# Performance work log

Hardware: AMD Instinct MI355X
Metric: run time of the kernel (lower is better)

## Reference

```python
import jax, jax.numpy as jnp
import numpy as np

NOISE_EPS = 1e-2   # Shazeer noisy-gating stddev floor
LN_EPS = 1e-6
LOSS_COEF = 0.01
K = 2              # num_activated_experts


def _layer_norm(x, w, b):
    mu = jnp.mean(x, axis=-1, keepdims=True)
    var = jnp.var(x, axis=-1, keepdims=True)
    return (x - mu) * jax.lax.rsqrt(var + LN_EPS) * w + b


def _cv_squared(v):
    return jnp.var(v) / (jnp.mean(v) ** 2 + 1e-10)


def _normal_cdf(z):
    return 0.5 * (1.0 + jax.scipy.special.erf(z / jnp.sqrt(jnp.asarray(2.0, z.dtype))))


def setup_inputs() -> dict:
    key = jax.random.key(0)
    ks = jax.random.split(key, 8)
    N, D, H, O, E = 8192, 512, 1024, 512, 8
    x = jax.random.normal(ks[0], (N, D), jnp.float32)
    x_offsets = jnp.sort(jax.random.randint(ks[1], (17,), 0, N)).astype(jnp.int64)
    noise = jax.random.normal(ks[2], (N, E), jnp.float32)
    s = 0.02
    return {
        "x": x,
        "x_offsets": x_offsets,
        "max_seq_len": 2048,
        "noise": noise,
        "norm_w": jnp.ones((D,), jnp.float32),
        "norm_bias": jnp.zeros((D,), jnp.float32),
        "w_gate": jax.random.normal(ks[3], (D, E), jnp.float32) * s,
        "w_noise": jax.random.normal(ks[4], (D, E), jnp.float32) * s,
        "W1": jax.random.normal(ks[5], (E, H, D), jnp.float32) * s,  # [E, model_d, input]
        "b1": jnp.zeros((E, H), jnp.float32),
        "W2": jax.random.normal(ks[6], (E, O, H), jnp.float32) * s,  # [E, output, model_d]
        "b2": jnp.zeros((E, O), jnp.float32),
        "output_weight": jax.random.normal(ks[7], (D, O), jnp.float32) * s,
    }


def reference(x, x_offsets, max_seq_len, noise, norm_w, norm_bias, w_gate, w_noise,
              W1, b1, W2, b2, output_weight):
    N, D = x.shape
    E = w_gate.shape[1]
    k_plus = min(K + 1, E)

    # pre-norm
    x_norm = _layer_norm(x, norm_w, norm_bias)

    # noisy top-k gating (training path)
    clean_logits = x_norm @ w_gate                      # [N, E]
    noise_stddev = jax.nn.softplus(x_norm @ w_noise) + NOISE_EPS
    noisy_logits = clean_logits + noise * noise_stddev

    top_logits, top_indices = jax.lax.top_k(noisy_logits, k_plus)   # [N, k+1]
    top_k_logits = top_logits[:, :K]
    top_k_indices = top_indices[:, :K]
    top_k_gates = jax.nn.softmax(top_k_logits, axis=-1)             # [N, K]

    rows = jnp.arange(N)[:, None]
    gates = jnp.zeros((N, E), top_k_gates.dtype).at[rows, top_k_indices].set(top_k_gates)

    # load = prob each expert is in top-k under the gating noise (Shazeer)
    flat = top_logits.reshape(-1)
    pos_in = jnp.arange(N) * k_plus + K
    thr_in = flat[pos_in][:, None]          # (k+1)-th value: threshold if already in
    thr_out = flat[pos_in - 1][:, None]     # k-th value: threshold if currently out
    is_in = noisy_logits > thr_in
    prob_in = _normal_cdf((clean_logits - thr_in) / noise_stddev)
    prob_out = _normal_cdf((clean_logits - thr_out) / noise_stddev)
    load_probs = jnp.where(is_in, prob_in, prob_out)                # [N, E]

    loss = LOSS_COEF * (_cv_squared(gates.sum(0)) + _cv_squared(load_probs.sum(0)))

    # dispatch stats: tokens per expert
    lengths = jnp.zeros((E,), jnp.float32).at[top_k_indices.reshape(-1)].add(1.0)
    load = lengths / lengths.sum()

    # grouped expert MLP (dense one-hot combine; gates are 0 for unrouted experts)
    h = jnp.einsum('nd,ehd->neh', x_norm, W1) + b1                  # [N, E, H]
    a = jax.nn.silu(h)
    y_e = jnp.einsum('neh,eoh->neo', a, W2) + b2                    # [N, E, O]
    y_moe = jnp.einsum('ne,neo->no', gates, y_e)                    # [N, O]

    # shared expert: addmm(y, shared_x=x, output_weight)
    y = y_moe + x @ output_weight
    return y, loss, load
```

## Files before the change

### kernel.cpp

```cpp
#include <hip/hip_runtime.h>
#include <math.h>

typedef unsigned short u16;
typedef unsigned int u32;

#define N_ROWS 8192
#define DDIM 512
#define HDIM 1024
#define ODIM 512
#define NEXP 8
#define MAXPAIRS (N_ROWS * 2)
#define MAXPOS (MAXPAIRS + NEXP * 128)
#define MAXTILES (MAXPOS / 128)

#define SM_CNT 0
#define SM_CUR 8
#define SM_AOFF 16
#define SM_GSUM 32
#define SM_LSUM 40
#define SM_WORDS 64

using short8 = __attribute__((ext_vector_type(8))) short;
using float4v = __attribute__((ext_vector_type(4))) float;

__device__ __forceinline__ u16 f2bf(float f) {
    union { float f; u32 u; } v; v.f = f;
    u32 u = v.u;
    return (u16)((u + 0x7fffu + ((u >> 16) & 1u)) >> 16);
}

__device__ __forceinline__ void async_copy16(u16* lds, const u16* g) {
    __builtin_amdgcn_global_load_lds(
        (const __attribute__((address_space(1))) void*)g,
        (__attribute__((address_space(3))) void*)lds, 16, 0, 0);
}

__global__ __launch_bounds__(512) void init1_kernel(int* small, float* zeropage) {
    int i = threadIdx.x;
    if (i < SM_WORDS) small[i] = 0;
    zeropage[i] = 0.f;
}

#define W1CONV_BLOCKS 4096
#define OWT_BLOCKS 256
#define BUCKET_BLOCKS 68
#define W2CONV_BLOCKS 2048
__global__ __launch_bounds__(256) void prep_kernel(
    const float* __restrict__ W1, const float* __restrict__ ow,
    const float* __restrict__ W2,
    u16* __restrict__ W1b, u16* __restrict__ owT, u16* __restrict__ W2b,
    int* __restrict__ bucket_rows)
{
    __shared__ __align__(16) float tile[32][33];
    int cb = blockIdx.x, tid = threadIdx.x;
    if (cb < W1CONV_BLOCKS) {
        size_t i = (size_t)cb * 256 + tid;
        float4 v = ((const float4*)W1)[i];
        ushort4 o;
        o.x = f2bf(v.x); o.y = f2bf(v.y); o.z = f2bf(v.z); o.w = f2bf(v.w);
        ((ushort4*)W1b)[i] = o;
    } else if (cb < W1CONV_BLOCKS + OWT_BLOCKS) {
        int t = cb - W1CONV_BLOCKS;
        int bx = (t & 15) * 32, by = (t >> 4) * 32;
        int tx = tid & 31, ty = tid >> 5;
        for (int r = ty; r < 32; r += 8) tile[r][tx] = ow[(size_t)(by + r) * ODIM + bx + tx];
        __syncthreads();
        for (int r = ty; r < 32; r += 8) owT[(size_t)(bx + r) * DDIM + by + tx] = f2bf(tile[tx][r]);
    } else if (cb < W1CONV_BLOCKS + OWT_BLOCKS + BUCKET_BLOCKS) {
        int i = (cb - W1CONV_BLOCKS - OWT_BLOCKS) * 256 + tid;
        if (i < MAXPOS) bucket_rows[i] = -1;
    } else {
        int j = cb - W1CONV_BLOCKS - OWT_BLOCKS - BUCKET_BLOCKS;
        size_t i = (size_t)j * 512 + tid;
#pragma unroll
        for (int t = 0; t < 2; t++, i += 256) {
            float4 v = ((const float4*)W2)[i];
            ushort4 o;
            o.x = f2bf(v.x); o.y = f2bf(v.y); o.z = f2bf(v.z); o.w = f2bf(v.w);
            ((ushort4*)W2b)[i] = o;
        }
    }
}

#define GATE_BLOCKS 512
__global__ __launch_bounds__(256) void gate_kernel(
    const float* __restrict__ x, const float* __restrict__ noise,
    const float* __restrict__ norm_w, const float* __restrict__ norm_b,
    const float* __restrict__ w_gate, const float* __restrict__ w_noise,
    u16* __restrict__ xnorm_bf, u16* __restrict__ x_bf,
    int* __restrict__ pair_expert, float* __restrict__ pair_gate,
    int* __restrict__ small)
{
    __shared__ __align__(16) float sh[2 * NEXP * DDIM + 16 * 17 + 32];
    float* wgT = sh;
    float* wnT = sh + NEXP * DDIM;
    float* lg = sh + 2 * NEXP * DDIM;
    float* blk_g = lg + 16 * 17;
    float* blk_l = blk_g + NEXP;
    int* blk_c = (int*)(blk_l + NEXP);
    float* smf = (float*)small;

    int b = blockIdx.x, tid = threadIdx.x;
    for (int i = tid; i < NEXP * DDIM; i += 256) {
        int d = i >> 3, e = i & 7;
        wgT[e * DDIM + d] = w_gate[i];
        wnT[e * DDIM + d] = w_noise[i];
    }
    if (tid < NEXP) { blk_g[tid] = 0.f; blk_l[tid] = 0.f; blk_c[tid] = 0; }
    __syncthreads();

    int wave = tid >> 6, lane = tid & 63;
    float nw[8], nb[8];
#pragma unroll
    for (int j = 0; j < 8; j++) { nw[j] = norm_w[j * 64 + lane]; nb[j] = norm_b[j * 64 + lane]; }

    bool l5 = (lane & 32) != 0, l4 = (lane & 16) != 0;
    bool l3 = (lane & 8) != 0, l2 = (lane & 4) != 0;

    for (int r = 0; r < 4; ++r) {
        int lrow16 = wave * 4 + r;
        int row = b * 16 + lrow16;
        const float* xr = x + (size_t)row * DDIM;
        float xv[8], s = 0.f, s2 = 0.f;
#pragma unroll
        for (int j = 0; j < 8; j++) { float v = xr[j * 64 + lane]; xv[j] = v; s += v; s2 += v * v; }
#pragma unroll
        for (int o = 32; o; o >>= 1) { s += __shfl_xor(s, o, 64); s2 += __shfl_xor(s2, o, 64); }
        float mu = s * (1.f / DDIM);
        float var = s2 * (1.f / DDIM) - mu * mu;
        float rstd = rsqrtf(var + 1e-6f);

        float acc[16];
#pragma unroll
        for (int e = 0; e < 16; e++) acc[e] = 0.f;
#pragma unroll
        for (int j = 0; j < 8; j++) {
            float v = (xv[j] - mu) * rstd * nw[j] + nb[j];
            int d = j * 64 + lane;
            xnorm_bf[(size_t)row * DDIM + d] = f2bf(v);
            x_bf[(size_t)row * DDIM + d] = f2bf(xv[j]);
#pragma unroll
            for (int e = 0; e < 8; e++) {
                acc[e] += v * wgT[e * DDIM + d];
                acc[8 + e] += v * wnT[e * DDIM + d];
            }
        }
        float t8[8];
#pragma unroll
        for (int v = 0; v < 8; v++) {
            float snd = l5 ? acc[v] : acc[v + 8];
            float kp = l5 ? acc[v + 8] : acc[v];
            t8[v] = kp + __shfl_xor(snd, 32, 64);
        }
        float t4[4];
#pragma unroll
        for (int v = 0; v < 4; v++) {
            float snd = l4 ? t8[v] : t8[v + 4];
            float kp = l4 ? t8[v + 4] : t8[v];
            t4[v] = kp + __shfl_xor(snd, 16, 64);
        }
        float t2[2];
#pragma unroll
        for (int v = 0; v < 2; v++) {
            float snd = l3 ? t4[v] : t4[v + 2];
            float kp = l3 ? t4[v + 2] : t4[v];
            t2[v] = kp + __shfl_xor(snd, 8, 64);
        }
        {
            float snd = l2 ? t2[0] : t2[1];
            float kp = l2 ? t2[1] : t2[0];
            float t1 = kp + __shfl_xor(snd, 4, 64);
            t1 += __shfl_xor(t1, 2, 64);
            t1 += __shfl_xor(t1, 1, 64);
            if ((lane & 3) == 0) lg[lrow16 * 17 + ((lane >> 2) & 15)] = t1;
        }
    }
    __syncthreads();

    if (tid < 16) {
        int row = b * 16 + tid;
        float cl[8], sd[8], nz[8];
#pragma unroll
        for (int e = 0; e < 8; e++) {
            cl[e] = lg[tid * 17 + e];
            float t = lg[tid * 17 + 8 + e];
            float sp = fmaxf(t, 0.f) + log1pf(expf(-fabsf(t)));
            sd[e] = sp + 0.01f;
            nz[e] = cl[e] + noise[(size_t)row * NEXP + e] * sd[e];
        }
        int idx[3]; float val[3]; u32 msk = 0;
#pragma unroll
        for (int t = 0; t < 3; t++) {
            float best = -INFINITY; int bi = 0;
#pragma unroll
            for (int e = 0; e < 8; e++)
                if (!((msk >> e) & 1) && nz[e] > best) { best = nz[e]; bi = e; }
            idx[t] = bi; val[t] = best; msk |= 1u << bi;
        }
        float e1 = expf(val[1] - val[0]);
        float g0 = 1.f / (1.f + e1), g1 = e1 / (1.f + e1);
        float thr_in = val[2], thr_out = val[1];

        pair_expert[row * 2] = idx[0]; pair_gate[row * 2] = g0;
        pair_expert[row * 2 + 1] = idx[1]; pair_gate[row * 2 + 1] = g1;
        atomicAdd(&blk_g[idx[0]], g0); atomicAdd(&blk_g[idx[1]], g1);
        atomicAdd(&blk_c[idx[0]], 1); atomicAdd(&blk_c[idx[1]], 1);
#pragma unroll
        for (int e = 0; e < 8; e++) {
            float thr = (nz[e] > thr_in) ? thr_in : thr_out;
            float z = (cl[e] - thr) / sd[e];
            float p = 0.5f * (1.f + erff(z * 0.70710678118654752f));
            atomicAdd(&blk_l[e], p);
        }
    }
    __syncthreads();
    if (tid < NEXP) {
        atomicAdd(smf + SM_GSUM + tid, blk_g[tid]);
        atomicAdd(smf + SM_LSUM + tid, blk_l[tid]);
        atomicAdd(&small[SM_CNT + tid], blk_c[tid]);
    }
}

__global__ __launch_bounds__(256) void scatter_kernel(
    const int* __restrict__ pair_expert, const float* __restrict__ pair_gate,
    int* __restrict__ small, int* __restrict__ bucket_rows, float* __restrict__ gate_by_pos,
    int* __restrict__ rowpos,
    float* __restrict__ out_loss, float* __restrict__ out_load)
{
    __shared__ int aoff[NEXP + 1];
    __shared__ int blk_cnt[NEXP];
    __shared__ int blk_base[NEXP];
    int tid = threadIdx.x;
    if (tid == 0) {
        int acc = 0; aoff[0] = 0;
        for (int e = 0; e < NEXP; e++) { acc += (small[SM_CNT + e] + 127) & ~127; aoff[e + 1] = acc; }
    }
    if (tid < NEXP) blk_cnt[tid] = 0;
    __syncthreads();
    int p = blockIdx.x * 256 + tid;
    int e = pair_expert[p];
    int local = atomicAdd(&blk_cnt[e], 1);
    __syncthreads();
    if (tid < NEXP)
        blk_base[tid] = aoff[tid] + atomicAdd(&small[SM_CUR + tid], blk_cnt[tid]);
    if (blockIdx.x == 0 && tid < NEXP + 1) small[SM_AOFF + tid] = aoff[tid];
    __syncthreads();
    int pos = blk_base[e] + local;
    bucket_rows[pos] = p >> 1;
    gate_by_pos[pos] = pair_gate[p];
    rowpos[p] = pos;

    if (blockIdx.x == 0 && tid == 0) {
        const float* gs = (const float*)small + SM_GSUM;
        const float* ls = (const float*)small + SM_LSUM;
        float cv[2];
        for (int t = 0; t < 2; t++) {
            const float* v = t ? ls : gs;
            float m = 0.f;
            for (int k = 0; k < NEXP; k++) m += v[k];
            m *= (1.f / NEXP);
            float var = 0.f;
            for (int k = 0; k < NEXP; k++) { float d = v[k] - m; var += d * d; }
            var *= (1.f / NEXP);
            cv[t] = var / (m * m + 1e-10f);
        }
        out_loss[0] = 0.01f * (cv[0] + cv[1]);
        int tot = 0;
        for (int k = 0; k < NEXP; k++) tot += small[SM_CNT + k];
        float inv = 1.f / (float)tot;
        for (int k = 0; k < NEXP; k++) out_load[k] = (float)small[SM_CNT + k] * inv;
    }
}

__global__ __launch_bounds__(256) void gemmA_kernel(
    const u16* __restrict__ xnorm, const u16* __restrict__ W1b,
    const u16* __restrict__ xbf, const u16* __restrict__ owT,
    const int* __restrict__ bucket_rows, const int* __restrict__ small,
    const float* __restrict__ b1, const u16* __restrict__ zeropage,
    u16* __restrict__ a_buf, float* __restrict__ y)
{
    constexpr int KD = 512;
    __shared__ __align__(16) u16 As[128 * 64];
    __shared__ __align__(16) u16 Bs[128 * 64];

    int tid = threadIdx.x;
    if (blockIdx.y >= 8) {
        int j = (blockIdx.y - 8) * 136 + blockIdx.x;
        if (j >= 256) return;
        int base = (j >> 2) * 128, bn = (j & 3) * 128;
        int wave = tid >> 6, lane = tid & 63;
        const int lrow = lane >> 2;
        const int kcol = (((lane & 3) ^ ((lane >> 3) & 3)) * 8);
        const int trow = wave * 32 + lrow;
        int wm = (wave & 1) * 64, wn = (wave >> 1) * 64;
        int fr = lane & 15, kq = lane >> 4;
        const int kg = ((kq ^ ((fr >> 1) & 3)) * 8);
        const u16* ga0 = xbf + (size_t)(base + trow) * KD + kcol;
        const u16* ga1 = xbf + (size_t)(base + trow + 16) * KD + kcol;
        const u16* gb0 = owT + (size_t)(bn + trow) * KD + kcol;
        const u16* gb1 = owT + (size_t)(bn + trow + 16) * KD + kcol;
        u16* As2 = (u16*)As; u16* Bs2 = (u16*)Bs;
        const int ofA0 = (wave * 32) * 32, ofA1 = (wave * 32 + 16) * 32;

        float4v acc[4][4];
#pragma unroll
        for (int i = 0; i < 4; i++)
#pragma unroll
            for (int jj = 0; jj < 4; jj++) acc[i][jj] = (float4v){0.f, 0.f, 0.f, 0.f};

        async_copy16(As2 + ofA0, ga0); async_copy16(As2 + ofA1, ga1);
        async_copy16(Bs2 + ofA0, gb0); async_copy16(Bs2 + ofA1, gb1);
        __syncthreads();
        int cur = 0;
        for (int t = 0; t < 16; ++t) {
            int nxt = cur ^ 1;
            if (t + 1 < 16) {
                int k1 = (t + 1) << 5;
                async_copy16(As2 + nxt * 4096 + ofA0, ga0 + k1);
                async_copy16(As2 + nxt * 4096 + ofA1, ga1 + k1);
                async_copy16(Bs2 + nxt * 4096 + ofA0, gb0 + k1);
                async_copy16(Bs2 + nxt * 4096 + ofA1, gb1 + k1);
            }
            short8 af[4], bf[4];
#pragma unroll
            for (int mt = 0; mt < 4; mt++) af[mt] = *(const short8*)&As2[cur * 4096 + (wm + mt * 16 + fr) * 32 + kg];
#pragma unroll
            for (int nt = 0; nt < 4; nt++) bf[nt] = *(const short8*)&Bs2[cur * 4096 + (wn + nt * 16 + fr) * 32 + kg];
#pragma unroll
            for (int mt = 0; mt < 4; mt++)
#pragma unroll
                for (int nt = 0; nt < 4; nt++)
                    acc[mt][nt] = __builtin_amdgcn_mfma_f32_16x16x32_bf16(af[mt], bf[nt], acc[mt][nt], 0, 0, 0);
            __syncthreads();
            cur = nxt;
        }
        int rbase = (lane >> 4) * 4, c16 = lane & 15;
#pragma unroll
        for (int mt = 0; mt < 4; mt++) {
            int gm = base + wm + mt * 16 + rbase;
#pragma unroll
            for (int nt = 0; nt < 4; nt++) {
                int gn = bn + wn + nt * 16 + c16;
#pragma unroll
                for (int r = 0; r < 4; r++)
                    y[(size_t)(gm + r) * ODIM + gn] = acc[mt][nt][r];
            }
        }
        return;
    }

    int base = blockIdx.x * 128;
    if (base >= small[SM_AOFF + 8]) return;
    int e = 0;
    while (e < 7 && base >= small[SM_AOFF + e + 1]) ++e;
    int bn = blockIdx.y * 128;
    const u16* Bsel = W1b + (size_t)e * HDIM * KD;

    int wave = tid >> 6, lane = tid & 63;
    int lr = lane >> 3;
    int lc = ((lane & 7) ^ lr) * 8;

    const u16* ga[4]; const u16* gb[4];
    u16* la[4]; u16* lb[4];
#pragma unroll
    for (int c = 0; c < 4; c++) {
        int tr = wave * 32 + c * 8;
        int r0 = bucket_rows[base + tr + lr];
        ga[c] = ((r0 < 0) ? zeropage : xnorm + (size_t)r0 * KD) + lc;
        gb[c] = Bsel + (size_t)(bn + tr + lr) * KD + lc;
        la[c] = &As[tr * 64];
        lb[c] = &Bs[tr * 64];
    }

    int wm = (wave & 1) * 64, wn = (wave >> 1) * 64;
    int fr = lane & 15, kq = lane >> 4, f7 = fr & 7;

    float4v acc[4][4];
#pragma unroll
    for (int i = 0; i < 4; i++)
#pragma unroll
        for (int j = 0; j < 4; j++) acc[i][j] = (float4v){0.f, 0.f, 0.f, 0.f};

    for (int k0 = 0; k0 < KD; k0 += 64) {
        __syncthreads();
#pragma unroll
        for (int c = 0; c < 4; c++) async_copy16(la[c], ga[c] + k0);
#pragma unroll
        for (int c = 0; c < 4; c++) async_copy16(lb[c], gb[c] + k0);
        __syncthreads();
        short8 af[4][2], bf[4][2];
#pragma unroll
        for (int mt = 0; mt < 4; mt++)
#pragma unroll
            for (int kh = 0; kh < 2; kh++)
                af[mt][kh] = *(const short8*)&As[(wm + mt * 16 + fr) * 64 + (((kq + 4 * kh) ^ f7) * 8)];
#pragma unroll
        for (int nt = 0; nt < 4; nt++)
#pragma unroll
            for (int kh = 0; kh < 2; kh++)
                bf[nt][kh] = *(const short8*)&Bs[(wn + nt * 16 + fr) * 64 + (((kq + 4 * kh) ^ f7) * 8)];
#pragma unroll
        for (int mt = 0; mt < 4; mt++)
#pragma unroll
            for (int nt = 0; nt < 4; nt++) {
                acc[mt][nt] = __builtin_amdgcn_mfma_f32_16x16x32_bf16(af[mt][0], bf[nt][0], acc[mt][nt], 0, 0, 0);
                acc[mt][nt] = __builtin_amdgcn_mfma_f32_16x16x32_bf16(af[mt][1], bf[nt][1], acc[mt][nt], 0, 0, 0);
            }
    }

    int rbase = (lane >> 4) * 4, c16 = lane & 15;
#pragma unroll
    for (int nt = 0; nt < 4; nt++) {
        int gn = bn + wn + nt * 16 + c16;
        float bv = b1[e * HDIM + gn];
#pragma unroll
        for (int mt = 0; mt < 4; mt++) {
            int gm = base + wm + mt * 16 + rbase;
#pragma unroll
            for (int r = 0; r < 4; r++) {
                float h = acc[mt][nt][r] + bv;
                float a = h * __builtin_amdgcn_rcpf(1.f + __expf(-h));
                a_buf[(size_t)(gm + r) * HDIM + gn] = f2bf(a);
            }
        }
    }
}

__global__ __launch_bounds__(512) void gemmB_kernel(
    const u16* __restrict__ a_buf, const u16* __restrict__ W2b,
    const int* __restrict__ bucket_rows, const int* __restrict__ small,
    const float* __restrict__ b2, const float* __restrict__ gate_by_pos,
    float* __restrict__ ye)
{
    constexpr int KD = 1024;
    __shared__ __align__(16) u16 As[2][128 * 32];
    __shared__ __align__(16) u16 Bs[2][256 * 32];

    int tid = threadIdx.x;
    int wave = tid >> 6, lane = tid & 63;
    const int lrow = lane >> 2;
    const int kcol = (((lane & 3) ^ ((lane >> 3) & 3)) * 8);
    int wm = (wave >> 2) * 64, wn = (wave & 3) * 64;
    int fr = lane & 15, kq = lane >> 4;
    const int kg = ((kq ^ ((fr >> 1) & 3)) * 8);

    int base = blockIdx.x * 128;
    if (base >= small[SM_AOFF + 8]) return;
    int e = 0;
    while (e < 7 && base >= small[SM_AOFF + e + 1]) ++e;
    int bn = blockIdx.y * 256;

    const u16* ga0 = a_buf + (size_t)(base + wave * 16 + lrow) * KD + kcol;
    const u16* Bsel = W2b + (size_t)e * ODIM * KD;
    const u16* gb0 = Bsel + (size_t)(bn + wave * 32 + lrow) * KD + kcol;
    const u16* gb1 = Bsel + (size_t)(bn + wave * 32 + 16 + lrow) * KD + kcol;
    const int ofA = (wave * 16) * 32;
    const int ofB0 = (wave * 32) * 32;
    const int ofB1 = (wave * 32 + 16) * 32;

    float4v acc[4][4];
#pragma unroll
    for (int i = 0; i < 4; i++)
#pragma unroll
        for (int j = 0; j < 4; j++) acc[i][j] = (float4v){0.f, 0.f, 0.f, 0.f};

    constexpr int nk = KD >> 5;
    async_copy16(&As[0][ofA], ga0);
    async_copy16(&Bs[0][ofB0], gb0);
    async_copy16(&Bs[0][ofB1], gb1);
    __syncthreads();

    int cur = 0;
    for (int t = 0; t < nk; ++t) {
        int nxt = cur ^ 1;
        if (t + 1 < nk) {
            int k1 = (t + 1) << 5;
            async_copy16(&As[nxt][ofA], ga0 + k1);
            async_copy16(&Bs[nxt][ofB0], gb0 + k1);
            async_copy16(&Bs[nxt][ofB1], gb1 + k1);
        }
        short8 af[4], bf[4];
#pragma unroll
        for (int mt = 0; mt < 4; mt++) af[mt] = *(const short8*)&As[cur][(wm + mt * 16 + fr) * 32 + kg];
#pragma unroll
        for (int nt = 0; nt < 4; nt++) bf[nt] = *(const short8*)&Bs[cur][(wn + nt * 16 + fr) * 32 + kg];
#pragma unroll
        for (int mt = 0; mt < 4; mt++)
#pragma unroll
            for (int nt = 0; nt < 4; nt++)
                acc[mt][nt] = __builtin_amdgcn_mfma_f32_16x16x32_bf16(af[mt], bf[nt], acc[mt][nt], 0, 0, 0);
        __syncthreads();
        cur = nxt;
    }

    int rbase = (lane >> 4) * 4, c16 = lane & 15;
#pragma unroll
    for (int mt = 0; mt < 4; mt++) {
        int pos0 = base + wm + mt * 16 + rbase;
        int rows[4]; float gs[4];
#pragma unroll
        for (int r = 0; r < 4; r++) { rows[r] = bucket_rows[pos0 + r]; gs[r] = gate_by_pos[pos0 + r]; }
#pragma unroll
        for (int nt = 0; nt < 4; nt++) {
            int gn = bn + wn + nt * 16 + c16;
            float b2v = b2[e * ODIM + gn];
#pragma unroll
            for (int r = 0; r < 4; r++) {
                if (rows[r] >= 0)
                    ye[(size_t)(pos0 + r) * ODIM + gn] = gs[r] * (acc[mt][nt][r] + b2v);
            }
        }
    }
}

__global__ __launch_bounds__(256) void combine_kernel(
    const float* __restrict__ ye, const int* __restrict__ rowpos,
    float* __restrict__ y)
{
    int tid = threadIdx.x;
    int row = blockIdx.x * 16 + (tid >> 4);
    int c0 = (tid & 15) * 32;
    int p0 = rowpos[row * 2];
    int p1 = rowpos[row * 2 + 1];
    const float4* e0 = (const float4*)(ye + (size_t)p0 * ODIM + c0);
    const float4* e1 = (const float4*)(ye + (size_t)p1 * ODIM + c0);
    float4* yp = (float4*)(y + (size_t)row * ODIM + c0);
#pragma unroll
    for (int i = 0; i < 8; i++) {
        float4 a = yp[i], b = e0[i], c = e1[i];
        a.x += b.x + c.x; a.y += b.y + c.y; a.z += b.z + c.z; a.w += b.w + c.w;
        yp[i] = a;
    }
}

extern "C" void kernel_launch(void* const* d_in, const int* in_sizes, int n_in,
                              void* d_out, int out_size, void* d_ws, size_t ws_size,
                              hipStream_t stream)
{
    (void)in_sizes; (void)n_in; (void)out_size; (void)ws_size;
    const float* x = (const float*)d_in[0];
    const float* noise = (const float*)d_in[3];
    const float* norm_w = (const float*)d_in[4];
    const float* norm_b = (const float*)d_in[5];
    const float* w_gate = (const float*)d_in[6];
    const float* w_noise = (const float*)d_in[7];
    const float* W1 = (const float*)d_in[8];
    const float* b1 = (const float*)d_in[9];
    const float* W2 = (const float*)d_in[10];
    const float* b2 = (const float*)d_in[11];
    const float* ow = (const float*)d_in[12];

    float* y = (float*)d_out;
    float* out_loss = y + (size_t)N_ROWS * ODIM;
    float* out_load = out_loss + 1;

    char* ws = (char*)d_ws;
    size_t off = 0;
    auto alloc = [&](size_t b) { size_t p = off; off = (off + b + 255) & ~(size_t)255; return p; };
    u16* xnorm_bf = (u16*)(ws + alloc((size_t)N_ROWS * DDIM * 2));
    u16* x_bf     = (u16*)(ws + alloc((size_t)N_ROWS * DDIM * 2));
    u16* W1b      = (u16*)(ws + alloc((size_t)NEXP * HDIM * DDIM * 2));
    u16* W2b      = (u16*)(ws + alloc((size_t)NEXP * ODIM * HDIM * 2));
    u16* owT      = (u16*)(ws + alloc((size_t)DDIM * ODIM * 2));
    u16* a_buf    = (u16*)(ws + alloc((size_t)MAXPOS * HDIM * 2));
    float* ye     = (float*)(ws + alloc((size_t)MAXPOS * ODIM * 4));
    int* pair_expert = (int*)(ws + alloc((size_t)MAXPAIRS * 4));
    float* pair_gate = (float*)(ws + alloc((size_t)MAXPAIRS * 4));
    float* gate_by_pos = (float*)(ws + alloc((size_t)MAXPOS * 4));
    int* bucket_rows = (int*)(ws + alloc((size_t)MAXPOS * 4));
    int* rowpos      = (int*)(ws + alloc((size_t)MAXPAIRS * 4));
    int* small       = (int*)(ws + alloc(SM_WORDS * 4));
    float* zeropage  = (float*)(ws + alloc(2048));

    init1_kernel<<<1, 512, 0, stream>>>(small, zeropage);
    prep_kernel<<<W1CONV_BLOCKS + OWT_BLOCKS + BUCKET_BLOCKS + W2CONV_BLOCKS, 256, 0, stream>>>(
        W1, ow, W2, W1b, owT, W2b, bucket_rows);
    gate_kernel<<<GATE_BLOCKS, 256, 0, stream>>>(
        x, noise, norm_w, norm_b, w_gate, w_noise,
        xnorm_bf, x_bf, pair_expert, pair_gate, small);
    scatter_kernel<<<MAXPAIRS / 256, 256, 0, stream>>>(pair_expert, pair_gate, small,
                                                       bucket_rows, gate_by_pos, rowpos,
                                                       out_loss, out_load);
    gemmA_kernel<<<dim3(MAXTILES, 8 + 2), 256, 0, stream>>>(xnorm_bf, W1b,
                                                            x_bf, owT, bucket_rows, small, b1,
                                                            (const u16*)zeropage, a_buf, y);
    gemmB_kernel<<<dim3(MAXTILES, 2), 512, 0, stream>>>(a_buf, W2b, bucket_rows,
                                                        small, b2, gate_by_pos, ye);
    combine_kernel<<<N_ROWS / 16, 256, 0, stream>>>(ye, rowpos, y);
}
```

Before: 249.5 us.

## Merge init, weight prep and gating into one kernel with per-block partial stats

Folds the init, weight-conversion and gating kernels into a single launch whose blocks split by index: gating blocks first, then W1/W2 bf16 conversion, the ow transpose and bucket init. Gating now reads w_gate/w_noise directly from global as float4 instead of staging them in LDS, and handles two rows at a time. Global atomics for per-expert sums are replaced by per-block partial arrays that the scatter kernel reduces. This removes two launches and the serial dependency between prep and gating. The cost is extra reduction work in scatter and redundant partial reads in every scatter block.

```diff
diff --git a/kernel.cpp b/kernel.cpp
--- a/kernel.cpp
+++ b/kernel.cpp
@@ -16,8 +16,6 @@
 #define SM_CNT 0
 #define SM_CUR 8
 #define SM_AOFF 16
-#define SM_GSUM 32
-#define SM_LSUM 40
 #define SM_WORDS 64
 
 using short8 = __attribute__((ext_vector_type(8))) short;
@@ -35,81 +33,75 @@
         (__attribute__((address_space(3))) void*)lds, 16, 0, 0);
 }
 
-__global__ __launch_bounds__(512) void init1_kernel(int* small, float* zeropage) {
-    int i = threadIdx.x;
-    if (i < SM_WORDS) small[i] = 0;
-    zeropage[i] = 0.f;
-}
-
-#define W1CONV_BLOCKS 4096
-#define OWT_BLOCKS 256
-#define BUCKET_BLOCKS 68
-#define W2CONV_BLOCKS 2048
-__global__ __launch_bounds__(256) void prep_kernel(
-    const float* __restrict__ W1, const float* __restrict__ ow,
-    const float* __restrict__ W2,
-    u16* __restrict__ W1b, u16* __restrict__ owT, u16* __restrict__ W2b,
-    int* __restrict__ bucket_rows)
-{
-    __shared__ __align__(16) float tile[32][33];
-    int cb = blockIdx.x, tid = threadIdx.x;
-    if (cb < W1CONV_BLOCKS) {
-        size_t i = (size_t)cb * 256 + tid;
-        float4 v = ((const float4*)W1)[i];
-        ushort4 o;
-        o.x = f2bf(v.x); o.y = f2bf(v.y); o.z = f2bf(v.z); o.w = f2bf(v.w);
-        ((ushort4*)W1b)[i] = o;
-    } else if (cb < W1CONV_BLOCKS + OWT_BLOCKS) {
-        int t = cb - W1CONV_BLOCKS;
-        int bx = (t & 15) * 32, by = (t >> 4) * 32;
-        int tx = tid & 31, ty = tid >> 5;
-        for (int r = ty; r < 32; r += 8) tile[r][tx] = ow[(size_t)(by + r) * ODIM + bx + tx];
-        __syncthreads();
-        for (int r = ty; r < 32; r += 8) owT[(size_t)(bx + r) * DDIM + by + tx] = f2bf(tile[tx][r]);
-    } else if (cb < W1CONV_BLOCKS + OWT_BLOCKS + BUCKET_BLOCKS) {
-        int i = (cb - W1CONV_BLOCKS - OWT_BLOCKS) * 256 + tid;
-        if (i < MAXPOS) bucket_rows[i] = -1;
-    } else {
-        int j = cb - W1CONV_BLOCKS - OWT_BLOCKS - BUCKET_BLOCKS;
-        size_t i = (size_t)j * 512 + tid;
-#pragma unroll
-        for (int t = 0; t < 2; t++, i += 256) {
-            float4 v = ((const float4*)W2)[i];
-            ushort4 o;
-            o.x = f2bf(v.x); o.y = f2bf(v.y); o.z = f2bf(v.z); o.w = f2bf(v.w);
-            ((ushort4*)W2b)[i] = o;
-        }
-    }
-}
-
-#define GATE_BLOCKS 512
-__global__ __launch_bounds__(256) void gate_kernel(
+#define MEGA_GATE 512
+#define MEGA_W1 2048
+#define MEGA_OWT 256
+#define MEGA_BUCKET 68
+#define MEGA_W2 2048
+#define MEGA_BLOCKS (MEGA_GATE + MEGA_W1 + MEGA_OWT + MEGA_BUCKET + MEGA_W2)
+__global__ __launch_bounds__(256) void mega_kernel(
     const float* __restrict__ x, const float* __restrict__ noise,
     const float* __restrict__ norm_w, const float* __restrict__ norm_b,
     const float* __restrict__ w_gate, const float* __restrict__ w_noise,
+    const float* __restrict__ W1, const float* __restrict__ ow,
+    const float* __restrict__ W2,
     u16* __restrict__ xnorm_bf, u16* __restrict__ x_bf,
     int* __restrict__ pair_expert, float* __restrict__ pair_gate,
-    int* __restrict__ small)
+    u16* __restrict__ W1b, u16* __restrict__ owT, u16* __restrict__ W2b,
+    int* __restrict__ bucket_rows, int* __restrict__ small, float* __restrict__ zeropage,
+    float* __restrict__ partial_g, float* __restrict__ partial_l, int* __restrict__ partial_c)
 {
-    __shared__ __align__(16) float sh[2 * NEXP * DDIM + 16 * 17 + 32];
-    float* wgT = sh;
-    float* wnT = sh + NEXP * DDIM;
-    float* lg = sh + 2 * NEXP * DDIM;
-    float* blk_g = lg + 16 * 17;
-    float* blk_l = blk_g + NEXP;
-    int* blk_c = (int*)(blk_l + NEXP);
-    float* smf = (float*)small;
-
+    __shared__ __align__(16) float sh[32 * 33 + 8];
     int b = blockIdx.x, tid = threadIdx.x;
-    for (int i = tid; i < NEXP * DDIM; i += 256) {
-        int d = i >> 3, e = i & 7;
-        wgT[e * DDIM + d] = w_gate[i];
-        wnT[e * DDIM + d] = w_noise[i];
-    }
-    if (tid < NEXP) { blk_g[tid] = 0.f; blk_l[tid] = 0.f; blk_c[tid] = 0; }
-    __syncthreads();
+
+    if (b >= MEGA_GATE) {
+        int cb = b - MEGA_GATE;
+        if (cb < MEGA_W1) {
+            size_t i = (size_t)cb * 512 + tid;
+#pragma unroll
+            for (int t = 0; t < 2; t++, i += 256) {
+                float4 v = ((const float4*)W1)[i];
+                ushort4 o;
+                o.x = f2bf(v.x); o.y = f2bf(v.y); o.z = f2bf(v.z); o.w = f2bf(v.w);
+                ((ushort4*)W1b)[i] = o;
+            }
+        } else if (cb < MEGA_W1 + MEGA_OWT) {
+            float (*tile)[33] = (float(*)[33])sh;
+            int t = cb - MEGA_W1;
+            int bx = (t & 15) * 32, by = (t >> 4) * 32;
+            int tx = tid & 31, ty = tid >> 5;
+            for (int r = ty; r < 32; r += 8) tile[r][tx] = ow[(size_t)(by + r) * ODIM + bx + tx];
+            __syncthreads();
+            for (int r = ty; r < 32; r += 8) owT[(size_t)(bx + r) * DDIM + by + tx] = f2bf(tile[tx][r]);
+        } else if (cb < MEGA_W1 + MEGA_OWT + MEGA_BUCKET) {
+            int lb = cb - MEGA_W1 - MEGA_OWT;
+            int i = lb * 256 + tid;
+            if (i < MAXPOS) bucket_rows[i] = -1;
+            if (lb == 0) {
+                if (tid < SM_WORDS) small[tid] = 0;
+                zeropage[tid] = 0.f; zeropage[tid + 256] = 0.f;
+            }
+        } else {
+            int j = cb - MEGA_W1 - MEGA_OWT - MEGA_BUCKET;
+            size_t i = (size_t)j * 512 + tid;
+#pragma unroll
+            for (int t = 0; t < 2; t++, i += 256) {
+                float4 v = ((const float4*)W2)[i];
+                ushort4 o;
+                o.x = f2bf(v.x); o.y = f2bf(v.y); o.z = f2bf(v.z); o.w = f2bf(v.w);
+                ((ushort4*)W2b)[i] = o;
+            }
+        }
+        return;
+    }
+
+    float* lg = sh;
+    float* blk_g = sh + 16 * 17;
+    float* blk_l = blk_g + 8;
+    int* blk_c = (int*)(blk_l + 8);
 
     int wave = tid >> 6, lane = tid & 63;
+    if (tid < 8) { blk_g[tid] = 0.f; blk_l[tid] = 0.f; blk_c[tid] = 0; }
     float nw[8], nb[8];
 #pragma unroll
     for (int j = 0; j < 8; j++) { nw[j] = norm_w[j * 64 + lane]; nb[j] = norm_b[j * 64 + lane]; }
@@ -117,56 +109,73 @@
     bool l5 = (lane & 32) != 0, l4 = (lane & 16) != 0;
     bool l3 = (lane & 8) != 0, l2 = (lane & 4) != 0;
 
-    for (int r = 0; r < 4; ++r) {
-        int lrow16 = wave * 4 + r;
-        int row = b * 16 + lrow16;
-        const float* xr = x + (size_t)row * DDIM;
-        float xv[8], s = 0.f, s2 = 0.f;
-#pragma unroll
-        for (int j = 0; j < 8; j++) { float v = xr[j * 64 + lane]; xv[j] = v; s += v; s2 += v * v; }
-#pragma unroll
-        for (int o = 32; o; o >>= 1) { s += __shfl_xor(s, o, 64); s2 += __shfl_xor(s2, o, 64); }
-        float mu = s * (1.f / DDIM);
-        float var = s2 * (1.f / DDIM) - mu * mu;
-        float rstd = rsqrtf(var + 1e-6f);
-
-        float acc[16];
-#pragma unroll
-        for (int e = 0; e < 16; e++) acc[e] = 0.f;
+    for (int half = 0; half < 2; ++half) {
+        float xv[2][8], mu[2], rstd[2];
+#pragma unroll
+        for (int r = 0; r < 2; ++r) {
+            int row = b * 16 + wave * 4 + half * 2 + r;
+            const float* xr = x + (size_t)row * DDIM;
+            float s = 0.f, s2 = 0.f;
+#pragma unroll
+            for (int j = 0; j < 8; j++) { float v = xr[j * 64 + lane]; xv[r][j] = v; s += v; s2 += v * v; }
+#pragma unroll
+            for (int o = 32; o; o >>= 1) { s += __shfl_xor(s, o, 64); s2 += __shfl_xor(s2, o, 64); }
+            mu[r] = s * (1.f / DDIM);
+            float var = s2 * (1.f / DDIM) - mu[r] * mu[r];
+            rstd[r] = rsqrtf(var + 1e-6f);
+        }
+        float acc[2][16];
+#pragma unroll
+        for (int r = 0; r < 2; ++r)
+#pragma unroll
+            for (int e = 0; e < 16; e++) acc[r][e] = 0.f;
 #pragma unroll
         for (int j = 0; j < 8; j++) {
-            float v = (xv[j] - mu) * rstd * nw[j] + nb[j];
             int d = j * 64 + lane;
-            xnorm_bf[(size_t)row * DDIM + d] = f2bf(v);
-            x_bf[(size_t)row * DDIM + d] = f2bf(xv[j]);
-#pragma unroll
-            for (int e = 0; e < 8; e++) {
-                acc[e] += v * wgT[e * DDIM + d];
-                acc[8 + e] += v * wnT[e * DDIM + d];
-            }
-        }
-        float t8[8];
-#pragma unroll
-        for (int v = 0; v < 8; v++) {
-            float snd = l5 ? acc[v] : acc[v + 8];
-            float kp = l5 ? acc[v + 8] : acc[v];
-            t8[v] = kp + __shfl_xor(snd, 32, 64);
-        }
-        float t4[4];
-#pragma unroll
-        for (int v = 0; v < 4; v++) {
-            float snd = l4 ? t8[v] : t8[v + 4];
-            float kp = l4 ? t8[v + 4] : t8[v];
-            t4[v] = kp + __shfl_xor(snd, 16, 64);
-        }
-        float t2[2];
-#pragma unroll
-        for (int v = 0; v < 2; v++) {
-            float snd = l3 ? t4[v] : t4[v + 2];
-            float kp = l3 ? t4[v + 2] : t4[v];
-            t2[v] = kp + __shfl_xor(snd, 8, 64);
-        }
-        {
+            float4 wg0 = *(const float4*)&w_gate[d * 8];
+            float4 wg1 = *(const float4*)&w_gate[d * 8 + 4];
+            float4 wn0 = *(const float4*)&w_noise[d * 8];
+            float4 wn1 = *(const float4*)&w_noise[d * 8 + 4];
+#pragma unroll
+            for (int r = 0; r < 2; ++r) {
+                int row = b * 16 + wave * 4 + half * 2 + r;
+                float v = (xv[r][j] - mu[r]) * rstd[r] * nw[j] + nb[j];
+                xnorm_bf[(size_t)row * DDIM + d] = f2bf(v);
+                x_bf[(size_t)row * DDIM + d] = f2bf(xv[r][j]);
+                acc[r][0] += v * wg0.x; acc[r][1] += v * wg0.y;
+                acc[r][2] += v * wg0.z; acc[r][3] += v * wg0.w;
+                acc[r][4] += v * wg1.x; acc[r][5] += v * wg1.y;
+                acc[r][6] += v * wg1.z; acc[r][7] += v * wg1.w;
+                acc[r][8] += v * wn0.x; acc[r][9] += v * wn0.y;
+                acc[r][10] += v * wn0.z; acc[r][11] += v * wn0.w;
+                acc[r][12] += v * wn1.x; acc[r][13] += v * wn1.y;
+                acc[r][14] += v * wn1.z; acc[r][15] += v * wn1.w;
+            }
+        }
+#pragma unroll
+        for (int r = 0; r < 2; ++r) {
+            int lrow16 = wave * 4 + half * 2 + r;
+            float t8[8];
+#pragma unroll
+            for (int v = 0; v < 8; v++) {
+                float snd = l5 ? acc[r][v] : acc[r][v + 8];
+                float kp = l5 ? acc[r][v + 8] : acc[r][v];
+                t8[v] = kp + __shfl_xor(snd, 32, 64);
+            }
+            float t4[4];
+#pragma unroll
+            for (int v = 0; v < 4; v++) {
+                float snd = l4 ? t8[v] : t8[v + 4];
+                float kp = l4 ? t8[v + 4] : t8[v];
+                t4[v] = kp + __shfl_xor(snd, 16, 64);
+            }
+            float t2[2];
+#pragma unroll
+            for (int v = 0; v < 2; v++) {
+                float snd = l3 ? t4[v] : t4[v + 2];
+                float kp = l3 ? t4[v + 2] : t4[v];
+                t2[v] = kp + __shfl_xor(snd, 8, 64);
+            }
             float snd = l2 ? t2[0] : t2[1];
             float kp = l2 ? t2[1] : t2[0];
             float t1 = kp + __shfl_xor(snd, 4, 64);
@@ -214,15 +223,17 @@
         }
     }
     __syncthreads();
-    if (tid < NEXP) {
-        atomicAdd(smf + SM_GSUM + tid, blk_g[tid]);
-        atomicAdd(smf + SM_LSUM + tid, blk_l[tid]);
-        atomicAdd(&small[SM_CNT + tid], blk_c[tid]);
+    if (tid < 8) {
+        partial_g[b * 8 + tid] = blk_g[tid];
+        partial_l[b * 8 + tid] = blk_l[tid];
+        partial_c[b * 8 + tid] = blk_c[tid];
     }
 }
 
 __global__ __launch_bounds__(256) void scatter_kernel(
     const int* __restrict__ pair_expert, const float* __restrict__ pair_gate,
+    const float* __restrict__ partial_g, const float* __restrict__ partial_l,
+    const int* __restrict__ partial_c,
     int* __restrict__ small, int* __restrict__ bucket_rows, float* __restrict__ gate_by_pos,
     int* __restrict__ rowpos,
     float* __restrict__ out_loss, float* __restrict__ out_load)
@@ -230,45 +241,77 @@
     __shared__ int aoff[NEXP + 1];
     __shared__ int blk_cnt[NEXP];
     __shared__ int blk_base[NEXP];
+    __shared__ int ired[256];
+    __shared__ float fred[256];
+    __shared__ float gsum[NEXP], lsum[NEXP];
     int tid = threadIdx.x;
+    int e = tid & 7, g = tid >> 3;
+
+    int s = 0;
+    for (int k = g; k < MEGA_GATE; k += 32) s += partial_c[k * 8 + e];
+    ired[tid] = s;
+    if (tid < NEXP) blk_cnt[tid] = 0;
+    __syncthreads();
+    if (tid < 64) ired[tid] = ired[tid] + ired[tid + 64] + ired[tid + 128] + ired[tid + 192];
+    __syncthreads();
+    if (tid < 8) {
+        int t = 0;
+        for (int q = tid; q < 64; q += 8) t += ired[q];
+        ired[tid] = t;
+    }
+    __syncthreads();
     if (tid == 0) {
         int acc = 0; aoff[0] = 0;
-        for (int e = 0; e < NEXP; e++) { acc += (small[SM_CNT + e] + 127) & ~127; aoff[e + 1] = acc; }
-    }
-    if (tid < NEXP) blk_cnt[tid] = 0;
-    __syncthreads();
+        for (int k = 0; k < NEXP; k++) { acc += (ired[k] + 127) & ~127; aoff[k + 1] = acc; }
+    }
+    __syncthreads();
+
     int p = blockIdx.x * 256 + tid;
-    int e = pair_expert[p];
-    int local = atomicAdd(&blk_cnt[e], 1);
+    int pe = pair_expert[p];
+    int local = atomicAdd(&blk_cnt[pe], 1);
     __syncthreads();
     if (tid < NEXP)
         blk_base[tid] = aoff[tid] + atomicAdd(&small[SM_CUR + tid], blk_cnt[tid]);
     if (blockIdx.x == 0 && tid < NEXP + 1) small[SM_AOFF + tid] = aoff[tid];
     __syncthreads();
-    int pos = blk_base[e] + local;
+    int pos = blk_base[pe] + local;
     bucket_rows[pos] = p >> 1;
     gate_by_pos[pos] = pair_gate[p];
     rowpos[p] = pos;
 
-    if (blockIdx.x == 0 && tid == 0) {
-        const float* gs = (const float*)small + SM_GSUM;
-        const float* ls = (const float*)small + SM_LSUM;
-        float cv[2];
-        for (int t = 0; t < 2; t++) {
-            const float* v = t ? ls : gs;
-            float m = 0.f;
-            for (int k = 0; k < NEXP; k++) m += v[k];
-            m *= (1.f / NEXP);
-            float var = 0.f;
-            for (int k = 0; k < NEXP; k++) { float d = v[k] - m; var += d * d; }
-            var *= (1.f / NEXP);
-            cv[t] = var / (m * m + 1e-10f);
-        }
-        out_loss[0] = 0.01f * (cv[0] + cv[1]);
-        int tot = 0;
-        for (int k = 0; k < NEXP; k++) tot += small[SM_CNT + k];
-        float inv = 1.f / (float)tot;
-        for (int k = 0; k < NEXP; k++) out_load[k] = (float)small[SM_CNT + k] * inv;
+    if (blockIdx.x == 0) {
+        float sg = 0.f, sl = 0.f;
+        for (int k = g; k < MEGA_GATE; k += 32) { sg += partial_g[k * 8 + e]; sl += partial_l[k * 8 + e]; }
+        fred[tid] = sg;
+        __syncthreads();
+        if (tid < 64) fred[tid] = fred[tid] + fred[tid + 64] + fred[tid + 128] + fred[tid + 192];
+        __syncthreads();
+        if (tid < 8) { float t = 0.f; for (int q = tid; q < 64; q += 8) t += fred[q]; gsum[tid] = t; }
+        __syncthreads();
+        fred[tid] = sl;
+        __syncthreads();
+        if (tid < 64) fred[tid] = fred[tid] + fred[tid + 64] + fred[tid + 128] + fred[tid + 192];
+        __syncthreads();
+        if (tid < 8) { float t = 0.f; for (int q = tid; q < 64; q += 8) t += fred[q]; lsum[tid] = t; }
+        __syncthreads();
+        if (tid == 0) {
+            float cv[2];
+            for (int t = 0; t < 2; t++) {
+                const float* v = t ? lsum : gsum;
+                float m = 0.f;
+                for (int k = 0; k < NEXP; k++) m += v[k];
+                m *= (1.f / NEXP);
+                float var = 0.f;
+                for (int k = 0; k < NEXP; k++) { float d = v[k] - m; var += d * d; }
+                var *= (1.f / NEXP);
+                cv[t] = var / (m * m + 1e-10f);
+            }
+            out_loss[0] = 0.01f * (cv[0] + cv[1]);
+            int tot = 0;
+            for (int k = 0; k < NEXP; k++) tot += ired[k];
+            float inv = 1.f / (float)tot;
+            for (int k = 0; k < NEXP; k++) out_load[k] = (float)ired[k] * inv;
+        }
     }
 }
 
@@ -571,15 +614,17 @@
     int* rowpos      = (int*)(ws + alloc((size_t)MAXPAIRS * 4));
     int* small       = (int*)(ws + alloc(SM_WORDS * 4));
     float* zeropage  = (float*)(ws + alloc(2048));
-
-    init1_kernel<<<1, 512, 0, stream>>>(small, zeropage);
-    prep_kernel<<<W1CONV_BLOCKS + OWT_BLOCKS + BUCKET_BLOCKS + W2CONV_BLOCKS, 256, 0, stream>>>(
-        W1, ow, W2, W1b, owT, W2b, bucket_rows);
-    gate_kernel<<<GATE_BLOCKS, 256, 0, stream>>>(
-        x, noise, norm_w, norm_b, w_gate, w_noise,
-        xnorm_bf, x_bf, pair_expert, pair_gate, small);
-    scatter_kernel<<<MAXPAIRS / 256, 256, 0, stream>>>(pair_expert, pair_gate, small,
-                                                       bucket_rows, gate_by_pos, rowpos,
+    float* partial_g = (float*)(ws + alloc((size_t)MEGA_GATE * NEXP * 4));
+    float* partial_l = (float*)(ws + alloc((size_t)MEGA_GATE * NEXP * 4));
+    int* partial_c   = (int*)(ws + alloc((size_t)MEGA_GATE * NEXP * 4));
+
+    mega_kernel<<<MEGA_BLOCKS, 256, 0, stream>>>(
+        x, noise, norm_w, norm_b, w_gate, w_noise, W1, ow, W2,
+        xnorm_bf, x_bf, pair_expert, pair_gate, W1b, owT, W2b,
+        bucket_rows, small, zeropage, partial_g, partial_l, partial_c);
+    scatter_kernel<<<MAXPAIRS / 256, 256, 0, stream>>>(pair_expert, pair_gate,
+                                                       partial_g, partial_l, partial_c,
+                                                       small, bucket_rows, gate_by_pos, rowpos,
                                                        out_loss, out_load);
     gemmA_kernel<<<dim3(MAXTILES, 8 + 2), 256, 0, stream>>>(xnorm_bf, W1b,
                                                             x_bf, owT, bucket_rows, small, b1,
```

Result: faster. 237.9 us (-4.6%).
